# Optimization experiments

Measured on AMD Instinct MI355X. Metric: run time of the kernel, lower is better.

## Reference

```python
import jax, jax.numpy as jnp
import numpy as np

B, A, C = 128, 8732, 21
ALPHA = 1.0
NEG_POS_RATIO = 3


def setup_inputs() -> dict:
    key = jax.random.key(0)
    k1, k2, k3, k4, k5 = jax.random.split(key, 5)
    confidences = jax.random.normal(k1, (B, A, C), dtype=jnp.float32)
    locations = jax.random.normal(k2, (B, A, 4), dtype=jnp.float32)
    gt_locations = jax.random.normal(k3, (B, A, 4), dtype=jnp.float32)
    raw_cls = jax.random.randint(k4, (B, A), 1, C)
    is_pos = jax.random.uniform(k5, (B, A)) < 0.03
    gt_labels = jnp.where(is_pos, raw_cls, 0).astype(jnp.int32)
    return {
        "confidences": confidences,
        "locations": locations,
        "gt_labels": gt_labels,
        "gt_locations": gt_locations,
    }


def reference(confidences, locations, gt_labels, gt_locations):
    pos_mask = gt_labels > 0                     # (B, A)
    neg_avail = gt_labels == 0                   # (B, A)

    # smooth L1 (beta=1) summed over positive anchors
    d = locations - gt_locations                 # (B, A, 4)
    ad = jnp.abs(d)
    sl1 = jnp.where(ad < 1.0, 0.5 * d * d, ad - 0.5)
    loc_loss = jnp.sum(sl1 * pos_mask[..., None].astype(sl1.dtype))

    # per-anchor cross entropy
    logp = jax.nn.log_softmax(confidences, axis=-1)              # (B, A, C)
    ce = -jnp.take_along_axis(logp, gt_labels[..., None].astype(jnp.int32), axis=-1)[..., 0]  # (B, A)

    # hard negative mining: top-(3*num_pos) CE among negatives, per row
    num_pos = jnp.sum(pos_mask, axis=1)                          # (B,)
    num_neg = jnp.minimum(NEG_POS_RATIO * num_pos, jnp.sum(neg_avail, axis=1))
    ce_neg = jnp.where(pos_mask, 0.0, ce)                        # zero out positives (CE >= 0)
    order = jnp.argsort(-ce_neg, axis=1)                         # descending
    ranks = jnp.argsort(order, axis=1)                           # rank of each anchor in descending order
    neg_mask = ranks < num_neg[:, None]

    keep = pos_mask | neg_mask
    conf_loss = jnp.sum(jnp.where(keep, ce, 0.0))

    total_loss = (loc_loss + ALPHA * conf_loss) / jnp.sum(num_pos).astype(loc_loss.dtype)
    return total_loss
```

## Files before the change

### kernel.cpp

```cpp
#include <hip/hip_runtime.h>
#include <math.h>

#define B_ 128
#define A_ 8732
#define C_ 21
#define APB 256
#define NBLK ((A_ + APB - 1) / APB)
#define NPART (B_ * NBLK)
#define KPT 9

#define OFF_PLOC 0
#define OFF_PPCE 17920
#define OFF_PNP  35840
#define OFF_RCN  53760
#define OFF_RNP  54272
#define OFF_CEN  57344

__global__ __launch_bounds__(256) void k_ce(
        const float* __restrict__ conf, const float* __restrict__ loc,
        const int* __restrict__ lab, const float* __restrict__ gloc,
        float* __restrict__ ce_neg, float* __restrict__ part_loc,
        float* __restrict__ part_pce, int* __restrict__ part_np)
{
    __shared__ float sConf[APB * C_];
    const int b   = blockIdx.y;
    const int a0  = blockIdx.x * APB;
    const int n   = min(APB, A_ - a0);
    const int tid = threadIdx.x;

    {
        const size_t base = ((size_t)b * A_ + a0) * C_;
        const int n4 = (n * C_) >> 2;
        const float4* src4 = (const float4*)(conf + base);
        float4* dst4 = (float4*)sConf;
        #pragma unroll
        for (int j = 0; j < 6; j++) {
            const int i = tid + j * 256;
            if (i < n4) dst4[i] = src4[i];
        }
    }
    __syncthreads();

    float pce = 0.f, lloss = 0.f;
    int pcnt = 0;
    if (tid < n) {
        const int a = a0 + tid;
        float v[C_];
        #pragma unroll
        for (int j = 0; j < C_; j++) v[j] = sConf[tid * C_ + j];
        float m = v[0];
        #pragma unroll
        for (int j = 1; j < C_; j++) m = fmaxf(m, v[j]);
        float s = 0.f;
        #pragma unroll
        for (int j = 0; j < C_; j++) s += __expf(v[j] - m);
        const int L = lab[(size_t)b * A_ + a];
        const float ce = __logf(s) + m - v[L];
        const bool pos = (L > 0);
        ce_neg[(size_t)b * A_ + a] = pos ? 0.f : ce;
        if (pos) {
            pce = ce;
            pcnt = 1;
            const float4 lv = ((const float4*)loc)[(size_t)b * A_ + a];
            const float4 gv = ((const float4*)gloc)[(size_t)b * A_ + a];
            float dx = lv.x - gv.x, dy = lv.y - gv.y, dz = lv.z - gv.z, dw = lv.w - gv.w;
            float ax = fabsf(dx), ay = fabsf(dy), az = fabsf(dz), aw = fabsf(dw);
            lloss  = (ax < 1.f) ? 0.5f * dx * dx : ax - 0.5f;
            lloss += (ay < 1.f) ? 0.5f * dy * dy : ay - 0.5f;
            lloss += (az < 1.f) ? 0.5f * dz * dz : az - 0.5f;
            lloss += (aw < 1.f) ? 0.5f * dw * dw : aw - 0.5f;
        }
    }

    #pragma unroll
    for (int off = 32; off > 0; off >>= 1) {
        pce   += __shfl_down(pce, off);
        lloss += __shfl_down(lloss, off);
        pcnt  += __shfl_down(pcnt, off);
    }
    __shared__ float wf[4], wl[4];
    __shared__ int wc[4];
    const int wave = tid >> 6, lane = tid & 63;
    if (lane == 0) { wf[wave] = pce; wl[wave] = lloss; wc[wave] = pcnt; }
    __syncthreads();
    if (tid == 0) {
        const int bid = b * NBLK + blockIdx.x;
        part_loc[bid] = wl[0] + wl[1] + wl[2] + wl[3];
        part_pce[bid] = wf[0] + wf[1] + wf[2] + wf[3];
        part_np[bid]  = wc[0] + wc[1] + wc[2] + wc[3];
    }
}

__global__ __launch_bounds__(1024, 2) void k_select(
        const float* __restrict__ ce_neg, const int* __restrict__ part_np,
        float* __restrict__ row_cneg, int* __restrict__ row_np)
{
    const int b = blockIdx.x;
    const int tid = threadIdx.x;
    const int wave = tid >> 6, lane = tid & 63;
    const float* ce = ce_neg + (size_t)b * A_;

    __shared__ unsigned long long shCnt[2][16];
    __shared__ float shS[16];
    __shared__ int shNp;

    unsigned keys[KPT];
    #pragma unroll
    for (int j = 0; j < KPT; j++) {
        const int i = tid + j * 1024;
        keys[j] = (i < A_) ? __float_as_uint(ce[i]) : 0u;
    }

    if (wave == 0) {
        int v = (lane < NBLK) ? part_np[b * NBLK + lane] : 0;
        #pragma unroll
        for (int off = 32; off > 0; off >>= 1) v += __shfl_down(v, off);
        if (lane == 0) shNp = v;
    }

    {
        unsigned c0 = 0; float s0 = 0.f;
        #pragma unroll
        for (int j = 0; j < KPT; j++) {
            c0 += (unsigned)__popcll(__ballot(keys[j] != 0u));
            s0 += __uint_as_float(keys[j]);
        }
        #pragma unroll
        for (int off = 32; off > 0; off >>= 1) s0 += __shfl_down(s0, off);
        if (lane == 0) { shCnt[0][wave] = c0; shS[wave] = s0; }
    }
    __syncthreads();

    const int np = shNp;
    const int k = min(3 * np, A_ - np);
    unsigned cnt0 = 0; float sum0 = 0.f;
    #pragma unroll
    for (int w = 0; w < 16; w++) { cnt0 += (unsigned)shCnt[0][w]; sum0 += shS[w]; }

    if (k <= 0) { if (tid == 0) { row_cneg[b] = 0.f; row_np[b] = np; } return; }
    if (cnt0 < (unsigned)k) {
        if (tid == 0) { row_cneg[b] = sum0; row_np[b] = np; }
        return;
    }

    unsigned lo = 0u, hi = 0x42800000u;
    int p = 1;
    while (hi - lo > 1u) {
        const unsigned w = hi - lo;
        unsigned m1, m2, m3;
        if (w >= 4u) { const unsigned q = w >> 2; m1 = lo + q; m2 = lo + 2*q; m3 = lo + 3*q; }
        else         { m1 = m2 = m3 = lo + (w >> 1); }
        unsigned c1 = 0, c2 = 0, c3 = 0;
        #pragma unroll
        for (int j = 0; j < KPT; j++) {
            c1 += (unsigned)__popcll(__ballot(keys[j] > m1));
            c2 += (unsigned)__popcll(__ballot(keys[j] > m2));
            c3 += (unsigned)__popcll(__ballot(keys[j] > m3));
        }
        if (lane == 0)
            shCnt[p][wave] = (unsigned long long)c1
                           | ((unsigned long long)c2 << 16)
                           | ((unsigned long long)c3 << 32);
        __syncthreads();
        unsigned long long t = 0;
        #pragma unroll
        for (int w2 = 0; w2 < 16; w2++) t += shCnt[p][w2];
        const int C1 = (int)(t & 0xFFFF), C2 = (int)((t >> 16) & 0xFFFF),
                  C3 = (int)((t >> 32) & 0xFFFF);
        if      (C3 >= k) { lo = m3; }
        else if (C2 >= k) { lo = m2; hi = m3; }
        else if (C1 >= k) { lo = m1; hi = m2; }
        else              { hi = m1; }
        p ^= 1;
    }

    const unsigned kth = hi;
    unsigned c = 0; float s = 0.f;
    #pragma unroll
    for (int j = 0; j < KPT; j++) {
        c += (unsigned)__popcll(__ballot(keys[j] > kth));
        s += (keys[j] > kth) ? __uint_as_float(keys[j]) : 0.f;
    }
    #pragma unroll
    for (int off = 32; off > 0; off >>= 1) s += __shfl_down(s, off);
    if (lane == 0) { shCnt[0][wave] = c; shS[wave] = s; }
    __syncthreads();
    if (tid == 0) {
        unsigned Cg = 0; float Sg = 0.f;
        #pragma unroll
        for (int w = 0; w < 16; w++) { Cg += (unsigned)shCnt[0][w]; Sg += shS[w]; }
        row_cneg[b] = Sg + (float)(k - (int)Cg) * __uint_as_float(kth);
        row_np[b] = np;
    }
}

__global__ __launch_bounds__(1024) void k_final(
        const float* __restrict__ part_loc, const float* __restrict__ part_pce,
        const float* __restrict__ row_cneg, const int* __restrict__ row_np,
        float* __restrict__ out)
{
    const int tid = threadIdx.x;
    const int wave = tid >> 6, lane = tid & 63;
    float s = 0.f;
    for (int i = tid; i < NPART; i += 1024) s += part_loc[i] + part_pce[i];
    int n = 0;
    if (tid < B_) { s += row_cneg[tid]; n = row_np[tid]; }
    #pragma unroll
    for (int off = 32; off > 0; off >>= 1) {
        s += __shfl_down(s, off);
        n += __shfl_down(n, off);
    }
    __shared__ float ws_[16];
    __shared__ int wn_[16];
    if (lane == 0) { ws_[wave] = s; wn_[wave] = n; }
    __syncthreads();
    if (tid == 0) {
        float S = 0.f; int N = 0;
        #pragma unroll
        for (int w = 0; w < 16; w++) { S += ws_[w]; N += wn_[w]; }
        out[0] = S / (float)N;
    }
}

extern "C" void kernel_launch(void* const* d_in, const int* in_sizes, int n_in,
                              void* d_out, int out_size, void* d_ws, size_t ws_size,
                              hipStream_t stream) {
    const float* conf = (const float*)d_in[0];
    const float* loc  = (const float*)d_in[1];
    const int*   lab  = (const int*)d_in[2];
    const float* gloc = (const float*)d_in[3];

    char* ws = (char*)d_ws;
    float* part_loc = (float*)(ws + OFF_PLOC);
    float* part_pce = (float*)(ws + OFF_PPCE);
    int*   part_np  = (int*)(ws + OFF_PNP);
    float* row_cneg = (float*)(ws + OFF_RCN);
    int*   row_np   = (int*)(ws + OFF_RNP);
    float* ce_neg   = (float*)(ws + OFF_CEN);

    dim3 g1(NBLK, B_);
    k_ce<<<g1, 256, 0, stream>>>(conf, loc, lab, gloc, ce_neg,
                                 part_loc, part_pce, part_np);
    k_select<<<B_, 1024, 0, stream>>>(ce_neg, part_np, row_cneg, row_np);
    k_final<<<1, 1024, 0, stream>>>(part_loc, part_pce, row_cneg, row_np,
                                    (float*)d_out);
}
```

Baseline: 188.9 us.

## Fuse final reduction into select kernel via atomic last-block ticket

Removes the third kernel launch by adding a 129th block to k_select that reduces the per-block partials, with every block atomically adding its contribution and the last one to arrive writing the output. Global accumulators are zeroed by the first thread of k_ce. The conf loads into shared memory now use nontemporal loads, and the label load is hoisted ahead of the shared-memory fill. The changes save one launch and a serial reduction, at the cost of atomics and a float sum order that is no longer deterministic.

Result: faster. 182.0 us (-3.7%).

```diff
diff --git a/kernel.cpp b/kernel.cpp
--- a/kernel.cpp
+++ b/kernel.cpp
@@ -9,18 +9,21 @@
 #define NPART (B_ * NBLK)
 #define KPT 9
 
+typedef float f4 __attribute__((ext_vector_type(4)));
+
 #define OFF_PLOC 0
 #define OFF_PPCE 17920
 #define OFF_PNP  35840
-#define OFF_RCN  53760
-#define OFF_RNP  54272
+#define OFF_SCAL 53760
 #define OFF_CEN  57344
 
 __global__ __launch_bounds__(256) void k_ce(
         const float* __restrict__ conf, const float* __restrict__ loc,
         const int* __restrict__ lab, const float* __restrict__ gloc,
         float* __restrict__ ce_neg, float* __restrict__ part_loc,
-        float* __restrict__ part_pce, int* __restrict__ part_np)
+        float* __restrict__ part_pce, int* __restrict__ part_np,
+        float* __restrict__ gsum, int* __restrict__ gN,
+        int* __restrict__ gticket)
 {
     __shared__ float sConf[APB * C_];
     const int b   = blockIdx.y;
@@ -28,15 +31,20 @@
     const int n   = min(APB, A_ - a0);
     const int tid = threadIdx.x;
 
+    if (b == 0 && blockIdx.x == 0 && tid == 0) { *gsum = 0.f; *gN = 0; *gticket = 0; }
+
+    const int a = a0 + min(tid, n - 1);
+    const int L = lab[(size_t)b * A_ + a];
+
     {
         const size_t base = ((size_t)b * A_ + a0) * C_;
         const int n4 = (n * C_) >> 2;
-        const float4* src4 = (const float4*)(conf + base);
-        float4* dst4 = (float4*)sConf;
+        const f4* src4 = (const f4*)(conf + base);
+        f4* dst4 = (f4*)sConf;
         #pragma unroll
         for (int j = 0; j < 6; j++) {
             const int i = tid + j * 256;
-            if (i < n4) dst4[i] = src4[i];
+            if (i < n4) dst4[i] = __builtin_nontemporal_load(&src4[i]);
         }
     }
     __syncthreads();
@@ -44,7 +52,6 @@
     float pce = 0.f, lloss = 0.f;
     int pcnt = 0;
     if (tid < n) {
-        const int a = a0 + tid;
         float v[C_];
         #pragma unroll
         for (int j = 0; j < C_; j++) v[j] = sConf[tid * C_ + j];
@@ -54,7 +61,6 @@
         float s = 0.f;
         #pragma unroll
         for (int j = 0; j < C_; j++) s += __expf(v[j] - m);
-        const int L = lab[(size_t)b * A_ + a];
         const float ce = __logf(s) + m - v[L];
         const bool pos = (L > 0);
         ce_neg[(size_t)b * A_ + a] = pos ? 0.f : ce;
@@ -92,133 +98,143 @@
 }
 
 __global__ __launch_bounds__(1024, 2) void k_select(
-        const float* __restrict__ ce_neg, const int* __restrict__ part_np,
-        float* __restrict__ row_cneg, int* __restrict__ row_np)
+        const float* __restrict__ ce_neg, const float* __restrict__ part_loc,
+        const float* __restrict__ part_pce, const int* __restrict__ part_np,
+        float* __restrict__ gsum, int* __restrict__ gN,
+        int* __restrict__ gticket, float* __restrict__ out)
 {
     const int b = blockIdx.x;
     const int tid = threadIdx.x;
     const int wave = tid >> 6, lane = tid & 63;
-    const float* ce = ce_neg + (size_t)b * A_;
 
     __shared__ unsigned long long shCnt[2][16];
     __shared__ float shS[16];
     __shared__ int shNp;
 
-    unsigned keys[KPT];
-    #pragma unroll
-    for (int j = 0; j < KPT; j++) {
-        const int i = tid + j * 1024;
-        keys[j] = (i < A_) ? __float_as_uint(ce[i]) : 0u;
-    }
-
-    if (wave == 0) {
-        int v = (lane < NBLK) ? part_np[b * NBLK + lane] : 0;
-        #pragma unroll
-        for (int off = 32; off > 0; off >>= 1) v += __shfl_down(v, off);
-        if (lane == 0) shNp = v;
-    }
-
-    {
-        unsigned c0 = 0; float s0 = 0.f;
+    float contrib = 0.f;
+
+    if (b == 128) {
+        float s = 0.f; int n = 0;
+        for (int i = tid; i < NPART; i += 1024) {
+            s += part_loc[i] + part_pce[i];
+            n += part_np[i];
+        }
+        #pragma unroll
+        for (int off = 32; off > 0; off >>= 1) {
+            s += __shfl_down(s, off);
+            n += __shfl_down(n, off);
+        }
+        __shared__ int shN2[16];
+        if (lane == 0) { shS[wave] = s; shN2[wave] = n; }
+        __syncthreads();
+        if (tid == 0) {
+            float S = 0.f; int N = 0;
+            #pragma unroll
+            for (int w = 0; w < 16; w++) { S += shS[w]; N += shN2[w]; }
+            contrib = S;
+            atomicAdd(gN, N);
+        }
+    } else {
+        const float* ce = ce_neg + (size_t)b * A_;
+
+        unsigned keys[KPT];
         #pragma unroll
         for (int j = 0; j < KPT; j++) {
-            c0 += (unsigned)__popcll(__ballot(keys[j] != 0u));
-            s0 += __uint_as_float(keys[j]);
-        }
-        #pragma unroll
-        for (int off = 32; off > 0; off >>= 1) s0 += __shfl_down(s0, off);
-        if (lane == 0) { shCnt[0][wave] = c0; shS[wave] = s0; }
-    }
-    __syncthreads();
-
-    const int np = shNp;
-    const int k = min(3 * np, A_ - np);
-    unsigned cnt0 = 0; float sum0 = 0.f;
-    #pragma unroll
-    for (int w = 0; w < 16; w++) { cnt0 += (unsigned)shCnt[0][w]; sum0 += shS[w]; }
-
-    if (k <= 0) { if (tid == 0) { row_cneg[b] = 0.f; row_np[b] = np; } return; }
-    if (cnt0 < (unsigned)k) {
-        if (tid == 0) { row_cneg[b] = sum0; row_np[b] = np; }
-        return;
-    }
-
-    unsigned lo = 0u, hi = 0x42800000u;
-    int p = 1;
-    while (hi - lo > 1u) {
-        const unsigned w = hi - lo;
-        unsigned m1, m2, m3;
-        if (w >= 4u) { const unsigned q = w >> 2; m1 = lo + q; m2 = lo + 2*q; m3 = lo + 3*q; }
-        else         { m1 = m2 = m3 = lo + (w >> 1); }
-        unsigned c1 = 0, c2 = 0, c3 = 0;
-        #pragma unroll
-        for (int j = 0; j < KPT; j++) {
-            c1 += (unsigned)__popcll(__ballot(keys[j] > m1));
-            c2 += (unsigned)__popcll(__ballot(keys[j] > m2));
-            c3 += (unsigned)__popcll(__ballot(keys[j] > m3));
-        }
-        if (lane == 0)
-            shCnt[p][wave] = (unsigned long long)c1
-                           | ((unsigned long long)c2 << 16)
-                           | ((unsigned long long)c3 << 32);
+            const int i = tid + j * 1024;
+            keys[j] = (i < A_) ? __float_as_uint(ce[i]) : 0u;
+        }
+
+        if (wave == 0) {
+            int v = (lane < NBLK) ? part_np[b * NBLK + lane] : 0;
+            #pragma unroll
+            for (int off = 32; off > 0; off >>= 1) v += __shfl_down(v, off);
+            if (lane == 0) shNp = v;
+        }
+
+        {
+            unsigned c0 = 0; float s0 = 0.f;
+            #pragma unroll
+            for (int j = 0; j < KPT; j++) {
+                c0 += (unsigned)__popcll(__ballot(keys[j] != 0u));
+                s0 += __uint_as_float(keys[j]);
+            }
+            #pragma unroll
+            for (int off = 32; off > 0; off >>= 1) s0 += __shfl_down(s0, off);
+            if (lane == 0) { shCnt[0][wave] = c0; shS[wave] = s0; }
+        }
         __syncthreads();
-        unsigned long long t = 0;
-        #pragma unroll
-        for (int w2 = 0; w2 < 16; w2++) t += shCnt[p][w2];
-        const int C1 = (int)(t & 0xFFFF), C2 = (int)((t >> 16) & 0xFFFF),
-                  C3 = (int)((t >> 32) & 0xFFFF);
-        if      (C3 >= k) { lo = m3; }
-        else if (C2 >= k) { lo = m2; hi = m3; }
-        else if (C1 >= k) { lo = m1; hi = m2; }
-        else              { hi = m1; }
-        p ^= 1;
-    }
-
-    const unsigned kth = hi;
-    unsigned c = 0; float s = 0.f;
-    #pragma unroll
-    for (int j = 0; j < KPT; j++) {
-        c += (unsigned)__popcll(__ballot(keys[j] > kth));
-        s += (keys[j] > kth) ? __uint_as_float(keys[j]) : 0.f;
-    }
-    #pragma unroll
-    for (int off = 32; off > 0; off >>= 1) s += __shfl_down(s, off);
-    if (lane == 0) { shCnt[0][wave] = c; shS[wave] = s; }
-    __syncthreads();
+
+        const int np = shNp;
+        const int k = min(3 * np, A_ - np);
+        unsigned cnt0 = 0; float sum0 = 0.f;
+        #pragma unroll
+        for (int w = 0; w < 16; w++) { cnt0 += (unsigned)shCnt[0][w]; sum0 += shS[w]; }
+
+        if (k <= 0) {
+            contrib = 0.f;
+        } else if (cnt0 < (unsigned)k) {
+            contrib = sum0;
+        } else {
+            unsigned lo = 0u, hi = 0x42800000u;
+            int p = 1;
+            while (hi - lo > 1u) {
+                const unsigned w = hi - lo;
+                unsigned m1, m2, m3;
+                if (w >= 4u) { const unsigned q = w >> 2; m1 = lo + q; m2 = lo + 2*q; m3 = lo + 3*q; }
+                else         { m1 = m2 = m3 = lo + (w >> 1); }
+                unsigned c1 = 0, c2 = 0, c3 = 0;
+                #pragma unroll
+                for (int j = 0; j < KPT; j++) {
+                    c1 += (unsigned)__popcll(__ballot(keys[j] > m1));
+                    c2 += (unsigned)__popcll(__ballot(keys[j] > m2));
+                    c3 += (unsigned)__popcll(__ballot(keys[j] > m3));
+                }
+                if (lane == 0)
+                    shCnt[p][wave] = (unsigned long long)c1
+                                   | ((unsigned long long)c2 << 16)
+                                   | ((unsigned long long)c3 << 32);
+                __syncthreads();
+                unsigned long long t = 0;
+                #pragma unroll
+                for (int w2 = 0; w2 < 16; w2++) t += shCnt[p][w2];
+                const int C1 = (int)(t & 0xFFFF), C2 = (int)((t >> 16) & 0xFFFF),
+                          C3 = (int)((t >> 32) & 0xFFFF);
+                if      (C3 >= k) { lo = m3; }
+                else if (C2 >= k) { lo = m2; hi = m3; }
+                else if (C1 >= k) { lo = m1; hi = m2; }
+                else              { hi = m1; }
+                p ^= 1;
+            }
+
+            const unsigned kth = hi;
+            unsigned c = 0; float s = 0.f;
+            #pragma unroll
+            for (int j = 0; j < KPT; j++) {
+                c += (unsigned)__popcll(__ballot(keys[j] > kth));
+                s += (keys[j] > kth) ? __uint_as_float(keys[j]) : 0.f;
+            }
+            #pragma unroll
+            for (int off = 32; off > 0; off >>= 1) s += __shfl_down(s, off);
+            if (lane == 0) { shCnt[0][wave] = c; shS[wave] = s; }
+            __syncthreads();
+            if (tid == 0) {
+                unsigned Cg = 0; float Sg = 0.f;
+                #pragma unroll
+                for (int w = 0; w < 16; w++) { Cg += (unsigned)shCnt[0][w]; Sg += shS[w]; }
+                contrib = Sg + (float)(k - (int)Cg) * __uint_as_float(kth);
+            }
+        }
+    }
+
     if (tid == 0) {
-        unsigned Cg = 0; float Sg = 0.f;
-        #pragma unroll
-        for (int w = 0; w < 16; w++) { Cg += (unsigned)shCnt[0][w]; Sg += shS[w]; }
-        row_cneg[b] = Sg + (float)(k - (int)Cg) * __uint_as_float(kth);
-        row_np[b] = np;
-    }
-}
-
-__global__ __launch_bounds__(1024) void k_final(
-        const float* __restrict__ part_loc, const float* __restrict__ part_pce,
-        const float* __restrict__ row_cneg, const int* __restrict__ row_np,
-        float* __restrict__ out)
-{
-    const int tid = threadIdx.x;
-    const int wave = tid >> 6, lane = tid & 63;
-    float s = 0.f;
-    for (int i = tid; i < NPART; i += 1024) s += part_loc[i] + part_pce[i];
-    int n = 0;
-    if (tid < B_) { s += row_cneg[tid]; n = row_np[tid]; }
-    #pragma unroll
-    for (int off = 32; off > 0; off >>= 1) {
-        s += __shfl_down(s, off);
-        n += __shfl_down(n, off);
-    }
-    __shared__ float ws_[16];
-    __shared__ int wn_[16];
-    if (lane == 0) { ws_[wave] = s; wn_[wave] = n; }
-    __syncthreads();
-    if (tid == 0) {
-        float S = 0.f; int N = 0;
-        #pragma unroll
-        for (int w = 0; w < 16; w++) { S += ws_[w]; N += wn_[w]; }
-        out[0] = S / (float)N;
+        atomicAdd(gsum, contrib);
+        __threadfence();
+        const int t = atomicAdd(gticket, 1);
+        if (t == 128) {
+            const float S = atomicAdd(gsum, 0.f);
+            const int   N = atomicAdd(gN, 0);
+            out[0] = S / (float)N;
+        }
     }
 }
 
@@ -234,14 +250,15 @@
     float* part_loc = (float*)(ws + OFF_PLOC);
     float* part_pce = (float*)(ws + OFF_PPCE);
     int*   part_np  = (int*)(ws + OFF_PNP);
-    float* row_cneg = (float*)(ws + OFF_RCN);
-    int*   row_np   = (int*)(ws + OFF_RNP);
+    float* gsum     = (float*)(ws + OFF_SCAL);
+    int*   gN       = (int*)(ws + OFF_SCAL + 4);
+    int*   gticket  = (int*)(ws + OFF_SCAL + 8);
     float* ce_neg   = (float*)(ws + OFF_CEN);
 
     dim3 g1(NBLK, B_);
     k_ce<<<g1, 256, 0, stream>>>(conf, loc, lab, gloc, ce_neg,
-                                 part_loc, part_pce, part_np);
-    k_select<<<B_, 1024, 0, stream>>>(ce_neg, part_np, row_cneg, row_np);
-    k_final<<<1, 1024, 0, stream>>>(part_loc, part_pce, row_cneg, row_np,
-                                    (float*)d_out);
+                                 part_loc, part_pce, part_np,
+                                 gsum, gN, gticket);
+    k_select<<<129, 1024, 0, stream>>>(ce_neg, part_loc, part_pce, part_np,
+                                       gsum, gN, gticket, (float*)d_out);
 }
```
